# Kernel optimization log

Measured on AMD Instinct MI355X. Metric: run time of the kernel, lower is better.

## Reference

```python
import jax, jax.numpy as jnp
from jax import lax
import numpy as np

B, T, NCLS, D = 64, 2048, 20, 2048
LCS_LEN, FSD_LEN = 64, 32
LAMB1, LAMB2, LAMB3 = 1.0, 5e-5, 8e-5
LAMB_LCS, LAMB_FSD = 0.01, 0.01
FEAT_MARGIN = 50.0
THRES = 0.5
GAMMA = 0.1


def cos_sim(a, b):
    a = a / jnp.linalg.norm(a, axis=1, keepdims=True)
    b = b / jnp.linalg.norm(b, axis=1, keepdims=True)
    return a @ b.T


def dp_fsd(c0, c1):
    # soft-LCS/DTW-style recurrence with maxGamma (soft max) over 3 neighbors
    h = c0.shape[-1] // 2
    m = cos_sim(c0[:, :h], c1[:, :h])  # [L, L]
    g = cos_sim(c0[:, h:], c1[:, h:])  # [L, L]
    L = m.shape[0]

    def row_step(prev_row, mg):
        m_row, g_row = mg
        diag = prev_row[:-1]  # C[i-1, j-1]
        up = prev_row[1:]     # C[i-1, j]

        def col_step(left, xs):  # left = C[i, j-1]
            d, u, mij, gij = xs
            neigh = jnp.stack([d, gij + u, gij + left])
            val = mij + GAMMA * jax.nn.logsumexp(neigh / GAMMA)
            return val, val

        _, row_vals = lax.scan(col_step, jnp.zeros((), m.dtype), (diag, up, m_row, g_row))
        new_row = jnp.concatenate([jnp.zeros((1,), m.dtype), row_vals])
        return new_row, None

    final_row, _ = lax.scan(row_step, jnp.zeros(L + 1, m.dtype), (m, g))
    return final_row[-1]


def dp_lcs(c0, c1):
    s = cos_sim(c0, c1)  # [L, L]
    L = s.shape[0]

    def row_step(prev_row, s_row):
        diag = prev_row[:-1]
        up = prev_row[1:]

        def col_step(left, xs):
            d, u, sij = xs
            val = jnp.where(sij > THRES, d + sij, jnp.maximum(u, left))
            return val, val

        _, row_vals = lax.scan(col_step, jnp.zeros((), s.dtype), (diag, up, s_row))
        return jnp.concatenate([jnp.zeros((1,), s.dtype), row_vals]), None

    final_row, _ = lax.scan(row_step, jnp.zeros(L + 1, s.dtype), s)
    return final_row[-1]


def cls_criterion(p, lab):
    return -jnp.mean(jnp.sum(jnp.log(p + 1e-10) * lab, axis=1))


def forward_once(ai_cls, ac_cls, ab_cls, vlab, att, ai_feat, ac_feat, ab_feat, ai_cas):
    bs = ai_cls.shape[0]
    ones = jnp.ones((bs, 1), ai_cls.dtype)
    zeros = jnp.zeros((bs, 1), ai_cls.dtype)
    inst_lab = jnp.concatenate([vlab, zeros], axis=1)
    cont_lab = jnp.concatenate([vlab, ones], axis=1)
    back_lab = jnp.concatenate([jnp.zeros_like(vlab), ones], axis=1)
    inst_lab = inst_lab / jnp.sum(inst_lab, axis=1, keepdims=True)
    cont_lab = cont_lab / jnp.sum(cont_lab, axis=1, keepdims=True)
    back_lab = back_lab / jnp.sum(back_lab, axis=1, keepdims=True)

    inst_loss = cls_criterion(ai_cls, inst_lab)
    cont_loss = cls_criterion(ac_cls, cont_lab)
    back_loss = cls_criterion(ab_cls, back_lab)

    guide_loss = jnp.mean(jnp.sum(jnp.abs(1.0 - ai_cas[:, :, -1] - lax.stop_gradient(att[:, :, 0])), axis=1))

    n_inst = jnp.linalg.norm(ai_feat, axis=1)
    n_cont = jnp.linalg.norm(ac_feat, axis=1)
    n_back = jnp.linalg.norm(ab_feat, axis=1)
    f1 = jnp.maximum(FEAT_MARGIN - n_inst + n_cont, 0.0)
    f2 = jnp.maximum(FEAT_MARGIN - n_cont + n_back, 0.0)
    f3 = n_back
    feat_loss = jnp.mean((f1 + f2 + f3) ** 2)

    sparse_loss = jnp.mean(jnp.sum(att[:, :, :2], axis=1))

    cls_loss = inst_loss + cont_loss + back_loss  # THUMOS14 weights 1/1/1
    return cls_loss + LAMB1 * guide_loss + LAMB2 * feat_loss + LAMB3 * sparse_loss


def _pair_loss(vals, pair_label):
    bs = vals.shape[0]
    pos = jnp.sum(vals * pair_label)
    neg = jnp.sum(vals * (1.0 - pair_label))
    pos_num = jnp.sum(pair_label)
    neg_num = bs - pos_num
    return neg / (neg_num + 1e-10) - pos / (pos_num + 1e-10)


def ftcl_forward(act_inst_cls_0, act_cont_cls_0, act_back_cls_0, vid_label_0, temp_att_0,
                 act_inst_feat_0, act_cont_feat_0, act_back_feat_0, act_inst_cas_0,
                 lcs_candi_0, fsd_act_candi_0, fsd_bak_candi_0,
                 act_inst_cls_1, act_cont_cls_1, act_back_cls_1, vid_label_1, temp_att_1,
                 act_inst_feat_1, act_cont_feat_1, act_back_feat_1, act_inst_cas_1,
                 lcs_candi_1, fsd_act_candi_1, fsd_bak_candi_1):
    loss_0 = forward_once(act_inst_cls_0, act_cont_cls_0, act_back_cls_0, vid_label_0, temp_att_0,
                          act_inst_feat_0, act_cont_feat_0, act_back_feat_0, act_inst_cas_0)
    loss_1 = forward_once(act_inst_cls_1, act_cont_cls_1, act_back_cls_1, vid_label_1, temp_att_1,
                          act_inst_feat_1, act_cont_feat_1, act_back_feat_1, act_inst_cas_1)
    acm_loss = (loss_0 + loss_1) / 2.0

    pair_label = (jnp.sum(vid_label_0 * vid_label_1, axis=1) > 0).astype(jnp.float32)  # [B]

    lcs = jax.vmap(dp_lcs)(lcs_candi_0, lcs_candi_1)  # [B]
    lcs_loss = _pair_loss(lcs, pair_label)

    # pair==1 -> act_1, pair==0 -> bak_1 (matches the per-sample branch in torch)
    fsd_c1 = jnp.where(pair_label[:, None, None] > 0, fsd_act_candi_1, fsd_bak_candi_1)
    fsd = jax.vmap(dp_fsd)(fsd_act_candi_0, fsd_c1)  # [B]
    fsd_loss = _pair_loss(fsd, pair_label)

    return acm_loss + LAMB_LCS * lcs_loss + LAMB_FSD * fsd_loss


def setup_inputs() -> dict:
    key = jax.random.key(0)
    ks = iter(jax.random.split(key, 32))
    rand = lambda s: jax.random.uniform(next(ks), s, jnp.float32)
    randn = lambda s: jax.random.normal(next(ks), s, jnp.float32)
    inp = {}
    for sfx in ('0', '1'):
        inp[f'act_inst_cls_{sfx}'] = rand((B, NCLS + 1))
        inp[f'act_cont_cls_{sfx}'] = rand((B, NCLS + 1))
        inp[f'act_back_cls_{sfx}'] = rand((B, NCLS + 1))
        inp[f'vid_label_{sfx}'] = jnp.ones((B, NCLS), jnp.float32)
        inp[f'temp_att_{sfx}'] = rand((B, T, 3))
        inp[f'act_inst_feat_{sfx}'] = randn((B, D))
        inp[f'act_cont_feat_{sfx}'] = randn((B, D))
        inp[f'act_back_feat_{sfx}'] = randn((B, D))
        inp[f'act_inst_cas_{sfx}'] = rand((B, T, NCLS + 1))
        inp[f'lcs_candi_{sfx}'] = randn((B, LCS_LEN, D))
        inp[f'fsd_act_candi_{sfx}'] = randn((B, FSD_LEN, D))
        inp[f'fsd_bak_candi_{sfx}'] = randn((B, FSD_LEN, D))
    return inp


def reference(act_inst_cls_0, act_cont_cls_0, act_back_cls_0, vid_label_0, temp_att_0,
              act_inst_feat_0, act_cont_feat_0, act_back_feat_0, act_inst_cas_0,
              lcs_candi_0, fsd_act_candi_0, fsd_bak_candi_0,
              act_inst_cls_1, act_cont_cls_1, act_back_cls_1, vid_label_1, temp_att_1,
              act_inst_feat_1, act_cont_feat_1, act_back_feat_1, act_inst_cas_1,
              lcs_candi_1, fsd_act_candi_1, fsd_bak_candi_1):
    return ftcl_forward(act_inst_cls_0, act_cont_cls_0, act_back_cls_0, vid_label_0, temp_att_0,
                        act_inst_feat_0, act_cont_feat_0, act_back_feat_0, act_inst_cas_0,
                        lcs_candi_0, fsd_act_candi_0, fsd_bak_candi_0,
                        act_inst_cls_1, act_cont_cls_1, act_back_cls_1, vid_label_1, temp_att_1,
                        act_inst_feat_1, act_cont_feat_1, act_back_feat_1, act_inst_cas_1,
                        lcs_candi_1, fsd_act_candi_1, fsd_bak_candi_1)
```

## Files before the change

### kernel.cpp

```cpp
#include <hip/hip_runtime.h>
#include <math.h>

#define Bn 64
#define Tn 2048
#define NCLS 20
#define Dn 2048
#define LCSL 64
#define FSDL 32

#define WS_LCS 0
#define WS_FSD 64
#define WS_NORM 128
#define WS_GS 512
#define WS_LSQ 1024
#define WS_FSQ 66560
#define WS_SPART 99328
#define WS_MG 2196480

__global__ __launch_bounds__(256) void mega_kernel(
    const float* __restrict__ lcs0, const float* __restrict__ lcs1,
    const float* __restrict__ fA0, const float* __restrict__ fA1,
    const float* __restrict__ fB1,
    const float* __restrict__ vid0, const float* __restrict__ vid1,
    const float* __restrict__ cas0, const float* __restrict__ att0,
    const float* __restrict__ cas1, const float* __restrict__ att1,
    const float* __restrict__ f0, const float* __restrict__ f1,
    const float* __restrict__ f2, const float* __restrict__ f3,
    const float* __restrict__ f4, const float* __restrict__ f5,
    float* __restrict__ ws) {
    __shared__ float tA[2176];
    __shared__ float tB[2176];
    const int t = threadIdx.x;
    const int bid = blockIdx.x;

    if (bid < 512) {
        const int b = bid >> 3, ks = bid & 7;
        const float* c0 = lcs0 + (size_t)b * LCSL * Dn + ks * 256;
        const float* c1 = lcs1 + (size_t)b * LCSL * Dn + ks * 256;
        const int ti = t >> 4, tj = t & 15;
        const int i0 = ti * 4, j0 = tj * 4;
        float acc[4][4] = {};
        float sqa0 = 0.f, sqa1 = 0.f, sqb0 = 0.f, sqb1 = 0.f;

        for (int kc = 0; kc < 256; kc += 32) {
            __syncthreads();
            #pragma unroll
            for (int l = 0; l < 2; ++l) {
                int idx4 = l * 256 + t;
                int row = idx4 >> 3;
                int kq = (idx4 & 7) * 4;
                float4 av = *(const float4*)(c0 + (size_t)row * Dn + kc + kq);
                float4 bv = *(const float4*)(c1 + (size_t)row * Dn + kc + kq);
                int rowx = row ^ kq;
                tA[(kq + 0) * 68 + rowx] = av.x;
                tA[(kq + 1) * 68 + rowx] = av.y;
                tA[(kq + 2) * 68 + rowx] = av.z;
                tA[(kq + 3) * 68 + rowx] = av.w;
                tB[(kq + 0) * 68 + rowx] = bv.x;
                tB[(kq + 1) * 68 + rowx] = bv.y;
                tB[(kq + 2) * 68 + rowx] = bv.z;
                tB[(kq + 3) * 68 + rowx] = bv.w;
                float sa = av.x * av.x + av.y * av.y + av.z * av.z + av.w * av.w;
                float sb = bv.x * bv.x + bv.y * bv.y + bv.z * bv.z + bv.w * bv.w;
                if (l == 0) { sqa0 += sa; sqb0 += sb; }
                else        { sqa1 += sa; sqb1 += sb; }
            }
            __syncthreads();
            #pragma unroll 8
            for (int k = 0; k < 32; ++k) {
                int sk = k & 28;
                float4 a4 = *(const float4*)&tA[k * 68 + (i0 ^ sk)];
                float4 b4 = *(const float4*)&tB[k * 68 + (j0 ^ sk)];
                float a[4] = {a4.x, a4.y, a4.z, a4.w};
                float bb[4] = {b4.x, b4.y, b4.z, b4.w};
                #pragma unroll
                for (int r = 0; r < 4; ++r)
                    #pragma unroll
                    for (int c = 0; c < 4; ++c)
                        acc[r][c] = fmaf(a[r], bb[c], acc[r][c]);
            }
        }
        float* dst = ws + WS_SPART + (size_t)(b * 8 + ks) * 4096;
        #pragma unroll
        for (int r = 0; r < 4; ++r) {
            float4 v = {acc[r][0], acc[r][1], acc[r][2], acc[r][3]};
            *(float4*)(dst + (i0 + r) * 64 + j0) = v;
        }
        #pragma unroll
        for (int m = 1; m < 8; m <<= 1) {
            sqa0 += __shfl_xor(sqa0, m);
            sqa1 += __shfl_xor(sqa1, m);
            sqb0 += __shfl_xor(sqb0, m);
            sqb1 += __shfl_xor(sqb1, m);
        }
        if ((t & 7) == 0) {
            int r0 = t >> 3;
            float* q = ws + WS_LSQ + (size_t)(b * 8 + ks) * 128;
            q[r0] = sqa0;
            q[r0 + 32] = sqa1;
            q[64 + r0] = sqb0;
            q[96 + r0] = sqb1;
        }
    } else if (bid < 1024) {
        const int q = bid - 512;
        const int b = q >> 3, half = (q >> 2) & 1, ks = q & 3;
        float ps = 0.f;
        for (int c = 0; c < NCLS; ++c) ps += vid0[b * NCLS + c] * vid1[b * NCLS + c];
        const float* base1 = (ps > 0.f) ? fA1 : fB1;
        const float* c0 = fA0 + (size_t)b * FSDL * Dn + half * 1024 + ks * 256;
        const float* c1 = base1 + (size_t)b * FSDL * Dn + half * 1024 + ks * 256;
        const int ti = t >> 4, tj = t & 15;
        const int i0 = ti * 2, j0 = tj * 2;
        float acc[2][2] = {};
        float sqa0 = 0.f, sqa1 = 0.f, sqb0 = 0.f, sqb1 = 0.f;

        for (int kc = 0; kc < 256; kc += 64) {
            __syncthreads();
            #pragma unroll
            for (int l = 0; l < 2; ++l) {
                int idx4 = l * 256 + t;
                int row = idx4 >> 4;
                int kq = (idx4 & 15) * 4;
                float4 av = *(const float4*)(c0 + (size_t)row * Dn + kc + kq);
                float4 bv = *(const float4*)(c1 + (size_t)row * Dn + kc + kq);
                {
                    int r0x = row ^ ((kq + 0) & 30);
                    int r1x = row ^ ((kq + 1) & 30);
                    int r2x = row ^ ((kq + 2) & 30);
                    int r3x = row ^ ((kq + 3) & 30);
                    tA[(kq + 0) * 34 + r0x] = av.x;
                    tA[(kq + 1) * 34 + r1x] = av.y;
                    tA[(kq + 2) * 34 + r2x] = av.z;
                    tA[(kq + 3) * 34 + r3x] = av.w;
                    tB[(kq + 0) * 34 + r0x] = bv.x;
                    tB[(kq + 1) * 34 + r1x] = bv.y;
                    tB[(kq + 2) * 34 + r2x] = bv.z;
                    tB[(kq + 3) * 34 + r3x] = bv.w;
                }
                float sa = av.x * av.x + av.y * av.y + av.z * av.z + av.w * av.w;
                float sb = bv.x * bv.x + bv.y * bv.y + bv.z * bv.z + bv.w * bv.w;
                if (l == 0) { sqa0 += sa; sqb0 += sb; }
                else        { sqa1 += sa; sqb1 += sb; }
            }
            __syncthreads();
            #pragma unroll 8
            for (int k = 0; k < 64; ++k) {
                int sk = k & 30;
                float2 a2 = *(const float2*)&tA[k * 34 + (i0 ^ sk)];
                float2 b2 = *(const float2*)&tB[k * 34 + (j0 ^ sk)];
                acc[0][0] = fmaf(a2.x, b2.x, acc[0][0]);
                acc[0][1] = fmaf(a2.x, b2.y, acc[0][1]);
                acc[1][0] = fmaf(a2.y, b2.x, acc[1][0]);
                acc[1][1] = fmaf(a2.y, b2.y, acc[1][1]);
            }
        }
        float* dst = ws + WS_MG + (size_t)((b * 2 + half) * 4 + ks) * 1024;
        #pragma unroll
        for (int r = 0; r < 2; ++r) {
            float2 v = {acc[r][0], acc[r][1]};
            *(float2*)(dst + (i0 + r) * 32 + j0) = v;
        }
        #pragma unroll
        for (int m = 1; m < 16; m <<= 1) {
            sqa0 += __shfl_xor(sqa0, m);
            sqa1 += __shfl_xor(sqa1, m);
            sqb0 += __shfl_xor(sqb0, m);
            sqb1 += __shfl_xor(sqb1, m);
        }
        if ((t & 15) == 0) {
            int r0 = t >> 4;
            float* qq = ws + WS_FSQ + (size_t)((b * 2 + half) * 4 + ks) * 64;
            qq[r0] = sqa0;
            qq[r0 + 16] = sqa1;
            qq[32 + r0] = sqb0;
            qq[48 + r0] = sqb1;
        }
    } else if (bid < 1152) {
        const int gb = bid - 1024;
        const int N = Bn * Tn;
        float g0 = 0.f, s0 = 0.f, g1 = 0.f, s1 = 0.f;
        for (int n = gb * 256 + t; n < 2 * N; n += 128 * 256) {
            int sfx = (n >= N);
            int m = sfx ? (n - N) : n;
            const float* cas = sfx ? cas1 : cas0;
            const float* att = sfx ? att1 : att0;
            float a0 = att[m * 3 + 0];
            float a1 = att[m * 3 + 1];
            float g = fabsf(1.0f - cas[m * (NCLS + 1) + NCLS] - a0);
            float s = a0 + a1;
            if (sfx) { g1 += g; s1 += s; } else { g0 += g; s0 += s; }
        }
        float vals[4] = {g0, s0, g1, s1};
        #pragma unroll
        for (int v = 0; v < 4; ++v) tA[v * 256 + t] = vals[v];
        __syncthreads();
        for (int o = 128; o; o >>= 1) {
            if (t < o) {
                #pragma unroll
                for (int v = 0; v < 4; ++v) tA[v * 256 + t] += tA[v * 256 + t + o];
            }
            __syncthreads();
        }
        if (t < 4) ws[WS_GS + gb * 4 + t] = tA[t * 256];
    } else {
        int R = (bid - 1152) * 4 + (t >> 6);
        int lane = t & 63;
        const float* arr[6] = {f0, f1, f2, f3, f4, f5};
        const float* p = arr[R >> 6] + (size_t)(R & 63) * Dn;
        float s = 0.f;
        #pragma unroll
        for (int qd = 0; qd < 8; ++qd) {
            float4 v = *(const float4*)(p + qd * 256 + lane * 4);
            s += v.x * v.x + v.y * v.y + v.z * v.z + v.w * v.w;
        }
        for (int off = 32; off; off >>= 1) s += __shfl_down(s, off);
        if (lane == 0) ws[WS_NORM + R] = sqrtf(s);
    }
}

__global__ __launch_bounds__(256) void dp_kernel(float* __restrict__ ws) {
    const int t = threadIdx.x;
    if (blockIdx.x < 64) {
        const int b = blockIdx.x;
        __shared__ float S[64 * 68];
        __shared__ float inv[128];
        if (t < 128) {
            float s = 0.f;
            #pragma unroll
            for (int ks = 0; ks < 8; ++ks)
                s += ws[WS_LSQ + (size_t)(b * 8 + ks) * 128 + t];
            inv[t] = 1.0f / sqrtf(s);
        }
        __syncthreads();
        const float* sp = ws + WS_SPART + (size_t)b * 32768;
        #pragma unroll
        for (int qd = 0; qd < 4; ++qd) {
            int idx4 = qd * 256 + t;
            int i = idx4 >> 4, j = (idx4 & 15) * 4;
            float4 v = {0.f, 0.f, 0.f, 0.f};
            #pragma unroll
            for (int ks = 0; ks < 8; ++ks) {
                float4 p = *(const float4*)(sp + (size_t)ks * 4096 + idx4 * 4);
                v.x += p.x; v.y += p.y; v.z += p.z; v.w += p.w;
            }
            float ri = inv[i];
            S[i * 68 + j + 0] = v.x * ri * inv[64 + j + 0];
            S[i * 68 + j + 1] = v.y * ri * inv[64 + j + 1];
            S[i * 68 + j + 2] = v.z * ri * inv[64 + j + 2];
            S[i * 68 + j + 3] = v.w * ri * inv[64 + j + 3];
        }
        __syncthreads();
        if (t < 64) {
            float prev = 0.f, prevprev = 0.f;
            float sval_next = S[t * 68 + 0];
            for (int d = 2; d <= 128; ++d) {
                float s = sval_next;
                int jn = d - t - 1;
                if (jn >= 0 && jn < 64) sval_next = S[t * 68 + jn];
                float up = __shfl_up(prev, 1);
                float dg = __shfl_up(prevprev, 1);
                if (t == 0) { up = 0.f; dg = 0.f; }
                int j = d - t - 1;
                float left = prev;
                float val = (s > 0.5f) ? (dg + s) : fmaxf(up, left);
                float cur = (j >= 1 && j <= 64) ? val : 0.f;
                prevprev = prev;
                prev = cur;
            }
            if (t == 63) ws[WS_LCS + b] = prev;
        }
    } else {
        const int b = blockIdx.x - 64;
        __shared__ float M[32 * 36], G[32 * 36];
        __shared__ float inv[128];
        if (t < 128) {
            int half = t >> 6, sub = t & 63;
            float s = 0.f;
            #pragma unroll
            for (int ks = 0; ks < 4; ++ks)
                s += ws[WS_FSQ + (size_t)((b * 2 + half) * 4 + ks) * 64 + sub];
            inv[t] = 1.0f / sqrtf(s);
        }
        __syncthreads();
        {
            int idx4 = t;
            int i = idx4 >> 3, j = (idx4 & 7) * 4;
            float4 vM = {0.f, 0.f, 0.f, 0.f}, vG = {0.f, 0.f, 0.f, 0.f};
            #pragma unroll
            for (int ks = 0; ks < 4; ++ks) {
                float4 pM = *(const float4*)(ws + WS_MG + (size_t)((b * 2 + 0) * 4 + ks) * 1024 + idx4 * 4);
                float4 pG = *(const float4*)(ws + WS_MG + (size_t)((b * 2 + 1) * 4 + ks) * 1024 + idx4 * 4);
                vM.x += pM.x; vM.y += pM.y; vM.z += pM.z; vM.w += pM.w;
                vG.x += pG.x; vG.y += pG.y; vG.z += pG.z; vG.w += pG.w;
            }
            float riM = inv[i], riG = inv[64 + i];
            M[i * 36 + j + 0] = vM.x * riM * inv[32 + j + 0];
            M[i * 36 + j + 1] = vM.y * riM * inv[32 + j + 1];
            M[i * 36 + j + 2] = vM.z * riM * inv[32 + j + 2];
            M[i * 36 + j + 3] = vM.w * riM * inv[32 + j + 3];
            G[i * 36 + j + 0] = vG.x * riG * inv[96 + j + 0];
            G[i * 36 + j + 1] = vG.y * riG * inv[96 + j + 1];
            G[i * 36 + j + 2] = vG.z * riG * inv[96 + j + 2];
            G[i * 36 + j + 3] = vG.w * riG * inv[96 + j + 3];
        }
        __syncthreads();
        if (t < 32) {
            float prev = 0.f, prevprev = 0.f;
            float m_next = M[t * 36 + 0], g_next = G[t * 36 + 0];
            for (int d = 2; d <= 64; ++d) {
                float m = m_next, g = g_next;
                int jn = d - t - 1;
                if (jn >= 0 && jn < 32) { m_next = M[t * 36 + jn]; g_next = G[t * 36 + jn]; }
                float up = __shfl_up(prev, 1);
                float dg = __shfl_up(prevprev, 1);
                if (t == 0) { up = 0.f; dg = 0.f; }
                int j = d - t - 1;
                float left = prev;
                float x0 = dg * 10.0f;
                float x1 = (g + up) * 10.0f;
                float x2 = (g + left) * 10.0f;
                float mx = fmaxf(x0, fmaxf(x1, x2));
                float lse = mx + __logf(__expf(x0 - mx) + __expf(x1 - mx) + __expf(x2 - mx));
                float val = m + 0.1f * lse;
                float cur = (j >= 1 && j <= 32) ? val : 0.f;
                prevprev = prev;
                prev = cur;
            }
            if (t == 31) ws[WS_FSD + b] = prev;
        }
    }
}

__device__ float block_reduce(float v, float* red, int t) {
    red[t] = v;
    __syncthreads();
    for (int o = 128; o; o >>= 1) {
        if (t < o) red[t] += red[t + o];
        __syncthreads();
    }
    float r = red[0];
    __syncthreads();
    return r;
}

__global__ __launch_bounds__(256) void final_kernel(
    const float* __restrict__ ai0, const float* __restrict__ ac0,
    const float* __restrict__ ab0, const float* __restrict__ vid0,
    const float* __restrict__ ai1, const float* __restrict__ ac1,
    const float* __restrict__ ab1, const float* __restrict__ vid1,
    const float* __restrict__ ws, float* __restrict__ out) {
    __shared__ float rs0[Bn], rs1[Bn], plsh[Bn];
    __shared__ float red[256];
    int t = threadIdx.x;
    if (t < Bn) {
        float s0 = 0.f, s1 = 0.f, pp = 0.f;
        for (int c = 0; c < NCLS; ++c) {
            float a = vid0[t * NCLS + c], bl = vid1[t * NCLS + c];
            s0 += a; s1 += bl; pp += a * bl;
        }
        rs0[t] = s0;
        rs1[t] = s1;
        plsh[t] = (pp > 0.f) ? 1.f : 0.f;
    }
    __syncthreads();

    float inst0 = 0.f, cont0 = 0.f, back0 = 0.f;
    float inst1 = 0.f, cont1 = 0.f, back1 = 0.f;
    for (int idx = t; idx < Bn * (NCLS + 1); idx += 256) {
        int b = idx / (NCLS + 1), c = idx % (NCLS + 1);
        float v0 = (c < NCLS) ? vid0[b * NCLS + c] : 0.f;
        float v1 = (c < NCLS) ? vid1[b * NCLS + c] : 0.f;
        float wI0 = (c < NCLS) ? (v0 / rs0[b]) : 0.f;
        float wC0 = ((c < NCLS) ? v0 : 1.f) / (rs0[b] + 1.f);
        float wI1 = (c < NCLS) ? (v1 / rs1[b]) : 0.f;
        float wC1 = ((c < NCLS) ? v1 : 1.f) / (rs1[b] + 1.f);
        inst0 += logf(ai0[idx] + 1e-10f) * wI0;
        cont0 += logf(ac0[idx] + 1e-10f) * wC0;
        inst1 += logf(ai1[idx] + 1e-10f) * wI1;
        cont1 += logf(ac1[idx] + 1e-10f) * wC1;
        if (c == NCLS) {
            back0 += logf(ab0[idx] + 1e-10f);
            back1 += logf(ab1[idx] + 1e-10f);
        }
    }
    float sInst0 = block_reduce(inst0, red, t);
    float sCont0 = block_reduce(cont0, red, t);
    float sBack0 = block_reduce(back0, red, t);
    float sInst1 = block_reduce(inst1, red, t);
    float sCont1 = block_reduce(cont1, red, t);
    float sBack1 = block_reduce(back1, red, t);

    float g0 = 0.f, s0v = 0.f, g1 = 0.f, s1v = 0.f;
    for (int i = t; i < 128; i += 256) {
        g0  += ws[WS_GS + i * 4 + 0];
        s0v += ws[WS_GS + i * 4 + 1];
        g1  += ws[WS_GS + i * 4 + 2];
        s1v += ws[WS_GS + i * 4 + 3];
    }
    float sG0 = block_reduce(g0, red, t);
    float sS0 = block_reduce(s0v, red, t);
    float sG1 = block_reduce(g1, red, t);
    float sS1 = block_reduce(s1v, red, t);

    float fv0 = 0.f, fv1 = 0.f;
    if (t < Bn) {
        const float* nm = ws + WS_NORM;
        {
            float ni = nm[0 * Bn + t], nc = nm[1 * Bn + t], nb = nm[2 * Bn + t];
            float f1 = fmaxf(50.0f - ni + nc, 0.f);
            float f2 = fmaxf(50.0f - nc + nb, 0.f);
            float f = f1 + f2 + nb;
            fv0 = f * f;
        }
        {
            float ni = nm[3 * Bn + t], nc = nm[4 * Bn + t], nb = nm[5 * Bn + t];
            float f1 = fmaxf(50.0f - ni + nc, 0.f);
            float f2 = fmaxf(50.0f - nc + nb, 0.f);
            float f = f1 + f2 + nb;
            fv1 = f * f;
        }
    }
    float sFeat0 = block_reduce(fv0, red, t) / (float)Bn;
    float sFeat1 = block_reduce(fv1, red, t) / (float)Bn;

    float posL = 0.f, negL = 0.f, posF = 0.f, negF = 0.f, pln = 0.f;
    if (t < Bn) {
        float pl = plsh[t];
        float lv = ws[WS_LCS + t];
        float fv = ws[WS_FSD + t];
        posL = lv * pl; negL = lv * (1.f - pl);
        posF = fv * pl; negF = fv * (1.f - pl);
        pln = pl;
    }
    float sPosL = block_reduce(posL, red, t);
    float sNegL = block_reduce(negL, red, t);
    float sPosF = block_reduce(posF, red, t);
    float sNegF = block_reduce(negF, red, t);
    float sPln = block_reduce(pln, red, t);

    if (t == 0) {
        float cls0 = -(sInst0 + sCont0 + sBack0) / (float)Bn;
        float cls1 = -(sInst1 + sCont1 + sBack1) / (float)Bn;
        float guide0 = sG0 / (float)Bn;
        float sparse0 = sS0 / (float)(Bn * 2);
        float guide1 = sG1 / (float)Bn;
        float sparse1 = sS1 / (float)(Bn * 2);
        float loss0 = cls0 + 1.0f * guide0 + 5e-05f * sFeat0 + 8e-05f * sparse0;
        float loss1 = cls1 + 1.0f * guide1 + 5e-05f * sFeat1 + 8e-05f * sparse1;
        float acm = 0.5f * (loss0 + loss1);
        float posn = sPln;
        float negn = (float)Bn - posn;
        float lcs_loss = sNegL / (negn + 1e-10f) - sPosL / (posn + 1e-10f);
        float fsd_loss = sNegF / (negn + 1e-10f) - sPosF / (posn + 1e-10f);
        out[0] = acm + 0.01f * lcs_loss + 0.01f * fsd_loss;
    }
}

extern "C" void kernel_launch(void* const* d_in, const int* in_sizes, int n_in,
                              void* d_out, int out_size, void* d_ws, size_t ws_size,
                              hipStream_t stream) {
    (void)in_sizes; (void)n_in; (void)out_size; (void)ws_size;
    const float* ai0  = (const float*)d_in[0];
    const float* ac0  = (const float*)d_in[1];
    const float* ab0  = (const float*)d_in[2];
    const float* vid0 = (const float*)d_in[3];
    const float* att0 = (const float*)d_in[4];
    const float* fi0  = (const float*)d_in[5];
    const float* fc0  = (const float*)d_in[6];
    const float* fb0  = (const float*)d_in[7];
    const float* cas0 = (const float*)d_in[8];
    const float* lcs0 = (const float*)d_in[9];
    const float* fsdA0 = (const float*)d_in[10];
    const float* ai1  = (const float*)d_in[12];
    const float* ac1  = (const float*)d_in[13];
    const float* ab1  = (const float*)d_in[14];
    const float* vid1 = (const float*)d_in[15];
    const float* att1 = (const float*)d_in[16];
    const float* fi1  = (const float*)d_in[17];
    const float* fc1  = (const float*)d_in[18];
    const float* fb1  = (const float*)d_in[19];
    const float* cas1 = (const float*)d_in[20];
    const float* lcs1 = (const float*)d_in[21];
    const float* fsdA1 = (const float*)d_in[22];
    const float* fsdB1 = (const float*)d_in[23];

    float* ws = (float*)d_ws;

    mega_kernel<<<1248, 256, 0, stream>>>(lcs0, lcs1, fsdA0, fsdA1, fsdB1,
                                          vid0, vid1, cas0, att0, cas1, att1,
                                          fi0, fc0, fb0, fi1, fc1, fb1, ws);
    dp_kernel<<<128, 256, 0, stream>>>(ws);
    final_kernel<<<1, 256, 0, stream>>>(ai0, ac0, ab0, vid0, ai1, ac1, ab1, vid1, ws,
                                        (float*)d_out);
}
```

Baseline: 244.3 us.

## Use bf16 MFMA for LCS/FSD similarity partial GEMMs with register prefetch

Replaces the scalar FMA outer-product loops that compute the partial cosine-similarity Gram matrices with bf16 MFMA 16x16x32 instructions. Inputs are converted to bf16 into XOR-swizzled row-major shared tiles. The next K chunk is prefetched into registers while the current one is stored to LDS. Squared norms are still accumulated in fp32, but the dot products lose precision to bf16, which could shift threshold decisions in the LCS DP.

```diff
diff --git a/kernel.cpp b/kernel.cpp
--- a/kernel.cpp
+++ b/kernel.cpp
@@ -7,6 +7,10 @@
 #define Dn 2048
 #define LCSL 64
 #define FSDL 32
+
+typedef __bf16 bf16x4 __attribute__((ext_vector_type(4)));
+typedef __bf16 bf16x8 __attribute__((ext_vector_type(8)));
+typedef float f32x4 __attribute__((ext_vector_type(4)));
 
 #define WS_LCS 0
 #define WS_FSD 64
@@ -28,152 +32,168 @@
     const float* __restrict__ f2, const float* __restrict__ f3,
     const float* __restrict__ f4, const float* __restrict__ f5,
     float* __restrict__ ws) {
-    __shared__ float tA[2176];
-    __shared__ float tB[2176];
+    __shared__ __bf16 tA[4096];
+    __shared__ __bf16 tB[4096];
     const int t = threadIdx.x;
     const int bid = blockIdx.x;
+    const int w = t >> 6, lane = t & 63;
+    const int quad = lane >> 4, l16 = lane & 15;
 
     if (bid < 512) {
         const int b = bid >> 3, ks = bid & 7;
         const float* c0 = lcs0 + (size_t)b * LCSL * Dn + ks * 256;
         const float* c1 = lcs1 + (size_t)b * LCSL * Dn + ks * 256;
-        const int ti = t >> 4, tj = t & 15;
-        const int i0 = ti * 4, j0 = tj * 4;
-        float acc[4][4] = {};
-        float sqa0 = 0.f, sqa1 = 0.f, sqb0 = 0.f, sqb1 = 0.f;
-
-        for (int kc = 0; kc < 256; kc += 32) {
+
+        f32x4 acc[4] = {};
+        float sqa[4] = {0.f, 0.f, 0.f, 0.f}, sqb[4] = {0.f, 0.f, 0.f, 0.f};
+        float4 pA[4], pB[4];
+        #pragma unroll
+        for (int l = 0; l < 4; ++l) {
+            int idx4 = l * 256 + t;
+            int row = idx4 >> 4, kq4 = idx4 & 15;
+            pA[l] = *(const float4*)(c0 + (size_t)row * Dn + kq4 * 4);
+            pB[l] = *(const float4*)(c1 + (size_t)row * Dn + kq4 * 4);
+        }
+        for (int kc = 0; kc < 4; ++kc) {
             __syncthreads();
             #pragma unroll
-            for (int l = 0; l < 2; ++l) {
+            for (int l = 0; l < 4; ++l) {
                 int idx4 = l * 256 + t;
-                int row = idx4 >> 3;
-                int kq = (idx4 & 7) * 4;
-                float4 av = *(const float4*)(c0 + (size_t)row * Dn + kc + kq);
-                float4 bv = *(const float4*)(c1 + (size_t)row * Dn + kc + kq);
-                int rowx = row ^ kq;
-                tA[(kq + 0) * 68 + rowx] = av.x;
-                tA[(kq + 1) * 68 + rowx] = av.y;
-                tA[(kq + 2) * 68 + rowx] = av.z;
-                tA[(kq + 3) * 68 + rowx] = av.w;
-                tB[(kq + 0) * 68 + rowx] = bv.x;
-                tB[(kq + 1) * 68 + rowx] = bv.y;
-                tB[(kq + 2) * 68 + rowx] = bv.z;
-                tB[(kq + 3) * 68 + rowx] = bv.w;
-                float sa = av.x * av.x + av.y * av.y + av.z * av.z + av.w * av.w;
-                float sb = bv.x * bv.x + bv.y * bv.y + bv.z * bv.z + bv.w * bv.w;
-                if (l == 0) { sqa0 += sa; sqb0 += sb; }
-                else        { sqa1 += sa; sqb1 += sb; }
+                int row = idx4 >> 4, kq4 = idx4 & 15;
+                int c = kq4 >> 1, h = kq4 & 1;
+                int pos = row * 64 + ((c ^ (row & 7)) << 3) + h * 4;
+                float4 av = pA[l], bv = pB[l];
+                bf16x4 a4 = {(__bf16)av.x, (__bf16)av.y, (__bf16)av.z, (__bf16)av.w};
+                bf16x4 b4 = {(__bf16)bv.x, (__bf16)bv.y, (__bf16)bv.z, (__bf16)bv.w};
+                *(bf16x4*)&tA[pos] = a4;
+                *(bf16x4*)&tB[pos] = b4;
+                sqa[l] += av.x * av.x + av.y * av.y + av.z * av.z + av.w * av.w;
+                sqb[l] += bv.x * bv.x + bv.y * bv.y + bv.z * bv.z + bv.w * bv.w;
+            }
+            if (kc < 3) {
+                const float* n0 = c0 + (kc + 1) * 64;
+                const float* n1 = c1 + (kc + 1) * 64;
+                #pragma unroll
+                for (int l = 0; l < 4; ++l) {
+                    int idx4 = l * 256 + t;
+                    int row = idx4 >> 4, kq4 = idx4 & 15;
+                    pA[l] = *(const float4*)(n0 + (size_t)row * Dn + kq4 * 4);
+                    pB[l] = *(const float4*)(n1 + (size_t)row * Dn + kq4 * 4);
+                }
             }
             __syncthreads();
-            #pragma unroll 8
-            for (int k = 0; k < 32; ++k) {
-                int sk = k & 28;
-                float4 a4 = *(const float4*)&tA[k * 68 + (i0 ^ sk)];
-                float4 b4 = *(const float4*)&tB[k * 68 + (j0 ^ sk)];
-                float a[4] = {a4.x, a4.y, a4.z, a4.w};
-                float bb[4] = {b4.x, b4.y, b4.z, b4.w};
+            #pragma unroll
+            for (int s = 0; s < 2; ++s) {
+                int ar = w * 16 + l16;
+                int ac_ = (s * 4 + quad) ^ (ar & 7);
+                bf16x8 af = *(const bf16x8*)&tA[ar * 64 + (ac_ << 3)];
                 #pragma unroll
-                for (int r = 0; r < 4; ++r)
-                    #pragma unroll
-                    for (int c = 0; c < 4; ++c)
-                        acc[r][c] = fmaf(a[r], bb[c], acc[r][c]);
+                for (int tj = 0; tj < 4; ++tj) {
+                    int br = tj * 16 + l16;
+                    int bc = (s * 4 + quad) ^ (br & 7);
+                    bf16x8 bf = *(const bf16x8*)&tB[br * 64 + (bc << 3)];
+                    acc[tj] = __builtin_amdgcn_mfma_f32_16x16x32_bf16(af, bf, acc[tj], 0, 0, 0);
+                }
             }
         }
         float* dst = ws + WS_SPART + (size_t)(b * 8 + ks) * 4096;
         #pragma unroll
-        for (int r = 0; r < 4; ++r) {
-            float4 v = {acc[r][0], acc[r][1], acc[r][2], acc[r][3]};
-            *(float4*)(dst + (i0 + r) * 64 + j0) = v;
-        }
-        #pragma unroll
-        for (int m = 1; m < 8; m <<= 1) {
-            sqa0 += __shfl_xor(sqa0, m);
-            sqa1 += __shfl_xor(sqa1, m);
-            sqb0 += __shfl_xor(sqb0, m);
-            sqb1 += __shfl_xor(sqb1, m);
-        }
-        if ((t & 7) == 0) {
-            int r0 = t >> 3;
-            float* q = ws + WS_LSQ + (size_t)(b * 8 + ks) * 128;
-            q[r0] = sqa0;
-            q[r0 + 32] = sqa1;
-            q[64 + r0] = sqb0;
-            q[96 + r0] = sqb1;
+        for (int tj = 0; tj < 4; ++tj)
+            #pragma unroll
+            for (int rg = 0; rg < 4; ++rg)
+                dst[(w * 16 + quad * 4 + rg) * 64 + tj * 16 + l16] = acc[tj][rg];
+        #pragma unroll
+        for (int l = 0; l < 4; ++l) {
+            float sa = sqa[l], sb = sqb[l];
+            #pragma unroll
+            for (int m = 1; m < 16; m <<= 1) {
+                sa += __shfl_xor(sa, m);
+                sb += __shfl_xor(sb, m);
+            }
+            if ((t & 15) == 0) {
+                int r = l * 16 + (t >> 4);
+                float* q = ws + WS_LSQ + (size_t)(b * 8 + ks) * 128;
+                q[r] = sa;
+                q[64 + r] = sb;
+            }
         }
     } else if (bid < 1024) {
-        const int q = bid - 512;
-        const int b = q >> 3, half = (q >> 2) & 1, ks = q & 3;
+        const int qb = bid - 512;
+        const int b = qb >> 3, half = (qb >> 2) & 1, ks = qb & 3;
         float ps = 0.f;
         for (int c = 0; c < NCLS; ++c) ps += vid0[b * NCLS + c] * vid1[b * NCLS + c];
         const float* base1 = (ps > 0.f) ? fA1 : fB1;
         const float* c0 = fA0 + (size_t)b * FSDL * Dn + half * 1024 + ks * 256;
         const float* c1 = base1 + (size_t)b * FSDL * Dn + half * 1024 + ks * 256;
-        const int ti = t >> 4, tj = t & 15;
-        const int i0 = ti * 2, j0 = tj * 2;
-        float acc[2][2] = {};
-        float sqa0 = 0.f, sqa1 = 0.f, sqb0 = 0.f, sqb1 = 0.f;
-
-        for (int kc = 0; kc < 256; kc += 64) {
+        const int wi = w >> 1, wj = w & 1;
+
+        f32x4 acc = {};
+        float sqa[2] = {0.f, 0.f}, sqb[2] = {0.f, 0.f};
+        float4 pA[2], pB[2];
+        #pragma unroll
+        for (int l = 0; l < 2; ++l) {
+            int idx4 = l * 256 + t;
+            int row = idx4 >> 4, kq4 = idx4 & 15;
+            pA[l] = *(const float4*)(c0 + (size_t)row * Dn + kq4 * 4);
+            pB[l] = *(const float4*)(c1 + (size_t)row * Dn + kq4 * 4);
+        }
+        for (int kc = 0; kc < 4; ++kc) {
             __syncthreads();
             #pragma unroll
             for (int l = 0; l < 2; ++l) {
                 int idx4 = l * 256 + t;
-                int row = idx4 >> 4;
-                int kq = (idx4 & 15) * 4;
-                float4 av = *(const float4*)(c0 + (size_t)row * Dn + kc + kq);
-                float4 bv = *(const float4*)(c1 + (size_t)row * Dn + kc + kq);
-                {
-                    int r0x = row ^ ((kq + 0) & 30);
-                    int r1x = row ^ ((kq + 1) & 30);
-                    int r2x = row ^ ((kq + 2) & 30);
-                    int r3x = row ^ ((kq + 3) & 30);
-                    tA[(kq + 0) * 34 + r0x] = av.x;
-                    tA[(kq + 1) * 34 + r1x] = av.y;
-                    tA[(kq + 2) * 34 + r2x] = av.z;
-                    tA[(kq + 3) * 34 + r3x] = av.w;
-                    tB[(kq + 0) * 34 + r0x] = bv.x;
-                    tB[(kq + 1) * 34 + r1x] = bv.y;
-                    tB[(kq + 2) * 34 + r2x] = bv.z;
-                    tB[(kq + 3) * 34 + r3x] = bv.w;
+                int row = idx4 >> 4, kq4 = idx4 & 15;
+                int c = kq4 >> 1, h = kq4 & 1;
+                int pos = row * 64 + ((c ^ (row & 7)) << 3) + h * 4;
+                float4 av = pA[l], bv = pB[l];
+                bf16x4 a4 = {(__bf16)av.x, (__bf16)av.y, (__bf16)av.z, (__bf16)av.w};
+                bf16x4 b4 = {(__bf16)bv.x, (__bf16)bv.y, (__bf16)bv.z, (__bf16)bv.w};
+                *(bf16x4*)&tA[pos] = a4;
+                *(bf16x4*)&tB[pos] = b4;
+                sqa[l] += av.x * av.x + av.y * av.y + av.z * av.z + av.w * av.w;
+                sqb[l] += bv.x * bv.x + bv.y * bv.y + bv.z * bv.z + bv.w * bv.w;
+            }
+            if (kc < 3) {
+                const float* n0 = c0 + (kc + 1) * 64;
+                const float* n1 = c1 + (kc + 1) * 64;
+                #pragma unroll
+                for (int l = 0; l < 2; ++l) {
+                    int idx4 = l * 256 + t;
+                    int row = idx4 >> 4, kq4 = idx4 & 15;
+                    pA[l] = *(const float4*)(n0 + (size_t)row * Dn + kq4 * 4);
+                    pB[l] = *(const float4*)(n1 + (size_t)row * Dn + kq4 * 4);
                 }
-                float sa = av.x * av.x + av.y * av.y + av.z * av.z + av.w * av.w;
-                float sb = bv.x * bv.x + bv.y * bv.y + bv.z * bv.z + bv.w * bv.w;
-                if (l == 0) { sqa0 += sa; sqb0 += sb; }
-                else        { sqa1 += sa; sqb1 += sb; }
             }
             __syncthreads();
-            #pragma unroll 8
-            for (int k = 0; k < 64; ++k) {
-                int sk = k & 30;
-                float2 a2 = *(const float2*)&tA[k * 34 + (i0 ^ sk)];
-                float2 b2 = *(const float2*)&tB[k * 34 + (j0 ^ sk)];
-                acc[0][0] = fmaf(a2.x, b2.x, acc[0][0]);
-                acc[0][1] = fmaf(a2.x, b2.y, acc[0][1]);
-                acc[1][0] = fmaf(a2.y, b2.x, acc[1][0]);
-                acc[1][1] = fmaf(a2.y, b2.y, acc[1][1]);
+            #pragma unroll
+            for (int s = 0; s < 2; ++s) {
+                int ar = wi * 16 + l16;
+                int ac_ = (s * 4 + quad) ^ (ar & 7);
+                bf16x8 af = *(const bf16x8*)&tA[ar * 64 + (ac_ << 3)];
+                int br = wj * 16 + l16;
+                int bc = (s * 4 + quad) ^ (br & 7);
+                bf16x8 bf = *(const bf16x8*)&tB[br * 64 + (bc << 3)];
+                acc = __builtin_amdgcn_mfma_f32_16x16x32_bf16(af, bf, acc, 0, 0, 0);
             }
         }
         float* dst = ws + WS_MG + (size_t)((b * 2 + half) * 4 + ks) * 1024;
         #pragma unroll
-        for (int r = 0; r < 2; ++r) {
-            float2 v = {acc[r][0], acc[r][1]};
-            *(float2*)(dst + (i0 + r) * 32 + j0) = v;
-        }
-        #pragma unroll
-        for (int m = 1; m < 16; m <<= 1) {
-            sqa0 += __shfl_xor(sqa0, m);
-            sqa1 += __shfl_xor(sqa1, m);
-            sqb0 += __shfl_xor(sqb0, m);
-            sqb1 += __shfl_xor(sqb1, m);
-        }
-        if ((t & 15) == 0) {
-            int r0 = t >> 4;
-            float* qq = ws + WS_FSQ + (size_t)((b * 2 + half) * 4 + ks) * 64;
-            qq[r0] = sqa0;
-            qq[r0 + 16] = sqa1;
-            qq[32 + r0] = sqb0;
-            qq[48 + r0] = sqb1;
+        for (int rg = 0; rg < 4; ++rg)
+            dst[(wi * 16 + quad * 4 + rg) * 32 + wj * 16 + l16] = acc[rg];
+        #pragma unroll
+        for (int l = 0; l < 2; ++l) {
+            float sa = sqa[l], sb = sqb[l];
+            #pragma unroll
+            for (int m = 1; m < 16; m <<= 1) {
+                sa += __shfl_xor(sa, m);
+                sb += __shfl_xor(sb, m);
+            }
+            if ((t & 15) == 0) {
+                int r = l * 16 + (t >> 4);
+                float* qq = ws + WS_FSQ + (size_t)((b * 2 + half) * 4 + ks) * 64;
+                qq[r] = sa;
+                qq[32 + r] = sb;
+            }
         }
     } else if (bid < 1152) {
         const int gb = bid - 1024;
@@ -190,21 +210,21 @@
             float s = a0 + a1;
             if (sfx) { g1 += g; s1 += s; } else { g0 += g; s0 += s; }
         }
+        float* red = (float*)tA;
         float vals[4] = {g0, s0, g1, s1};
         #pragma unroll
-        for (int v = 0; v < 4; ++v) tA[v * 256 + t] = vals[v];
+        for (int v = 0; v < 4; ++v) red[v * 256 + t] = vals[v];
         __syncthreads();
         for (int o = 128; o; o >>= 1) {
             if (t < o) {
                 #pragma unroll
-                for (int v = 0; v < 4; ++v) tA[v * 256 + t] += tA[v * 256 + t + o];
+                for (int v = 0; v < 4; ++v) red[v * 256 + t] += red[v * 256 + t + o];
             }
             __syncthreads();
         }
-        if (t < 4) ws[WS_GS + gb * 4 + t] = tA[t * 256];
+        if (t < 4) ws[WS_GS + gb * 4 + t] = red[t * 256];
     } else {
-        int R = (bid - 1152) * 4 + (t >> 6);
-        int lane = t & 63;
+        int R = (bid - 1152) * 4 + w;
         const float* arr[6] = {f0, f1, f2, f3, f4, f5};
         const float* p = arr[R >> 6] + (size_t)(R & 63) * Dn;
         float s = 0.f;
```

Result: no change. 240.6 us (-1.5%).
